# Kernel tuning notes

Measured on AMD Instinct MI355X. Metric: run time of the kernel, lower is better.

Reference implementation:

```python
import jax, jax.numpy as jnp
import numpy as np

N, D, E = 16384, 2048, 64   # tokens, d_model, num_experts
K = 9                        # self.k = min(k+1, num_experts) with k=8
EPS = 0.01
SIGMA = 1.0 / E              # Normal(0, 1/num_experts) stddev


def setup_inputs() -> dict:
    key = jax.random.key(0)
    ks = jax.random.split(key, 6)
    x = jax.random.normal(ks[0], (N, D), jnp.float32)
    Wr = jax.random.normal(ks[1], (D, E), jnp.float32) * 0.02
    br = jnp.zeros((E,), jnp.float32)
    Wn = jax.random.normal(ks[2], (D, E), jnp.float32) * 0.02
    bn = jnp.zeros((E,), jnp.float32)
    noise_eps = jax.random.normal(ks[3], (N, E), jnp.float32)
    # torch: (-empty.exponential_()).log() -> log of Exp(1) samples
    gumbel_noise = jnp.log(jax.random.exponential(ks[4], (N, E), jnp.float32))
    return {"x": x, "Wr": Wr, "br": br, "Wn": Wn, "bn": bn,
            "noise_eps": noise_eps, "gumbel_noise": gumbel_noise}


def reference(x, Wr, br, Wn, bn, noise_eps, gumbel_noise):
    raw_logits = x @ Wr + br                              # [N, E]
    noise_stddev = jax.nn.softplus(x @ Wn + bn) + EPS     # [N, E]
    noisy_logits = raw_logits + noise_eps * noise_stddev  # [N, E]

    top_vals, top_idx = jax.lax.top_k(noisy_logits, K)    # [N, K] sorted desc
    # scatter ones at top-k indices (indices unique per row)
    hard_mask = jax.nn.one_hot(top_idx, E, dtype=noisy_logits.dtype).sum(axis=1)  # [N, E]

    # gumbel-softmax straight-through relaxation
    mask_soft = jax.nn.softmax(noisy_logits + gumbel_noise, axis=-1)
    expert_mask = hard_mask - jax.lax.stop_gradient(mask_soft) + mask_soft

    route_prob = jax.nn.softmax(noisy_logits, axis=-1)    # [N, E]
    importance = jax.nn.softmax(raw_logits, axis=-1).sum(axis=0)  # [E]

    # load: P(raw + noise > threshold), Normal(0, 1/E) CDF per original
    threshold = top_vals[:, K - 1]                        # [N]
    z = (threshold[:, None] - raw_logits) / noise_stddev  # [N, E]
    cdf = 0.5 * (1.0 + jax.scipy.special.erf(z / (SIGMA * jnp.sqrt(jnp.float32(2.0)))))
    load = (1.0 - cdf).sum(axis=0)                        # [E]

    return (expert_mask, route_prob, importance, load)
```

## Files before the change

kernel.cpp:

```cpp
#include <hip/hip_runtime.h>
#include <hip/hip_bf16.h>
#include <math.h>

#define N_TOK 16384
#define DIM   2048
#define NE    64
#define TOPK  9

#define ROWS     32
#define DC       64
#define NCHUNK   (DIM / DC)
#define NTHREADS 256

typedef short  short8  __attribute__((ext_vector_type(8)));
typedef float  float4_ __attribute__((ext_vector_type(4)));
typedef unsigned short ushort_t;

__device__ __forceinline__ void async16(const void* g, void* l) {
    __builtin_amdgcn_global_load_lds(
        (const __attribute__((address_space(1))) void*)g,
        (__attribute__((address_space(3))) void*)l, 16, 0, 0);
}

__device__ __forceinline__ unsigned pk2(float a, float b) {
    float2 f; f.x = a; f.y = b;
    __hip_bfloat162 h = __float22bfloat162_rn(f);
    unsigned u;
    __builtin_memcpy(&u, &h, 4);
    return u;
}

__device__ __forceinline__ void cvt8(const float4_ va, const float4_ vb,
                                     short8* h, short8* l) {
    union { short8 s; unsigned u[4]; } H, L;
    const float f[8] = {va[0], va[1], va[2], va[3], vb[0], vb[1], vb[2], vb[3]};
#pragma unroll
    for (int i = 0; i < 4; ++i) {
        const float a = f[2 * i], b = f[2 * i + 1];
        const unsigned p = pk2(a, b);
        H.u[i] = p;
        const float ha = __uint_as_float(p << 16);
        const float hb = __uint_as_float(p & 0xffff0000u);
        L.u[i] = pk2(a - ha, b - hb);
    }
    *h = H.s; *l = L.s;
}

__device__ __forceinline__ float wave_max64(float v) {
#pragma unroll
    for (int off = 32; off > 0; off >>= 1)
        v = fmaxf(v, __shfl_xor(v, off, 64));
    return v;
}
__device__ __forceinline__ float wave_sum64(float v) {
#pragma unroll
    for (int off = 32; off > 0; off >>= 1)
        v += __shfl_xor(v, off, 64);
    return v;
}

__global__ __launch_bounds__(256)
void prep_w(const float* __restrict__ Wr, const float* __restrict__ Wn,
            ushort_t* __restrict__ wsW)
{
    const int gid = blockIdx.x * 256 + threadIdx.x;
    const int l   = gid & 63;
    const int ct  = (gid >> 6) & 7;
    const int kcg = gid >> 9;
    const int n   = ct * 16 + (l & 15);
    const int k0  = kcg * 32 + (l >> 4) * 8;
    const float* src = (n < NE) ? (Wr + n) : (Wn + (n - NE));
    union { short8 s; ushort_t us[8]; } H, L;
#pragma unroll
    for (int j = 0; j < 8; ++j) {
        const float v = src[(size_t)(k0 + j) * NE];
        const unsigned uv = __float_as_uint(v);
        const unsigned hb = (uv + 0x7fffu + ((uv >> 16) & 1u)) & 0xffff0000u;
        const float lo = v - __uint_as_float(hb);
        const unsigned ul = __float_as_uint(lo);
        H.us[j] = (ushort_t)(hb >> 16);
        L.us[j] = (ushort_t)((ul + 0x7fffu + ((ul >> 16) & 1u)) >> 16);
    }
    const size_t s0 = (size_t)(kcg * 8 + ct) * 2;
    *(short8*)(wsW + s0 * 512 + l * 8)         = H.s;
    *(short8*)(wsW + (s0 + 1) * 512 + l * 8)   = L.s;
}

__global__ __launch_bounds__(NTHREADS, 3)
void moe_main(const float* __restrict__ x,
              const float* __restrict__ br,
              const float* __restrict__ bn,
              const float* __restrict__ noise_eps,
              const float* __restrict__ gumbel,
              const ushort_t* __restrict__ wsW,
              float* __restrict__ out)
{
    __shared__ __align__(16) float smem[4352];

    const int t    = threadIdx.x;
    const int lane = t & 63;
    const int w    = t >> 6;
    const int c4   = lane & 15;
    const int q    = lane >> 4;
    const int row0 = blockIdx.x * ROWS;

    const float* gxp[2];
    int lxo[2];
#pragma unroll
    for (int ii = 0; ii < 2; ++ii) {
        const int i  = 2 * w + ii;
        const int r  = 4 * i + q;
        const int gk = c4 ^ (r & 15);
        gxp[ii] = x + (size_t)(row0 + r) * DIM + gk * 4;
        lxo[ii] = i * 256;
    }

    int aoff[2][2];
#pragma unroll
    for (int kc = 0; kc < 2; ++kc) {
        const int g0 = kc * 8 + q * 2;
        aoff[kc][0] = c4 * 64 + ((g0 ^ c4) * 4);
        aoff[kc][1] = c4 * 64 + (((g0 + 1) ^ c4) * 4);
    }

    float4_ acc[2][2];
#pragma unroll
    for (int rt = 0; rt < 2; ++rt)
#pragma unroll
        for (int cc = 0; cc < 2; ++cc)
            acc[rt][cc] = (float4_)(0.f);

    const char* wsB = (const char*)wsW;

#pragma unroll
    for (int ii = 0; ii < 2; ++ii) { async16(gxp[ii], &smem[lxo[ii]]); gxp[ii] += DC; }

    for (int ch = 0; ch < NCHUNK; ++ch) {
        __syncthreads();
        const int b = ch & 1;
        short8 bh[2][2], bl[2][2];
#pragma unroll
        for (int kc = 0; kc < 2; ++kc)
#pragma unroll
            for (int cc = 0; cc < 2; ++cc) {
                const size_t off = (size_t)(((ch * 2 + kc) * 8) + 2 * w + cc) * 2048 + lane * 16;
                bh[kc][cc] = *(const short8*)(wsB + off);
                bl[kc][cc] = *(const short8*)(wsB + off + 1024);
            }
        if (ch + 1 < NCHUNK) {
#pragma unroll
            for (int ii = 0; ii < 2; ++ii) {
                async16(gxp[ii], &smem[(b ^ 1) * 2048 + lxo[ii]]);
                gxp[ii] += DC;
            }
        }
        const float* xb = &smem[b * 2048];
#pragma unroll
        for (int kc = 0; kc < 2; ++kc)
#pragma unroll
            for (int rt = 0; rt < 2; ++rt) {
                const float4_ va = *(const float4_*)(xb + rt * 1024 + aoff[kc][0]);
                const float4_ vb = *(const float4_*)(xb + rt * 1024 + aoff[kc][1]);
                short8 ah, al;
                cvt8(va, vb, &ah, &al);
#pragma unroll
                for (int cc = 0; cc < 2; ++cc) {
                    acc[rt][cc] = __builtin_amdgcn_mfma_f32_16x16x32_bf16(ah, bh[kc][cc], acc[rt][cc], 0, 0, 0);
                    acc[rt][cc] = __builtin_amdgcn_mfma_f32_16x16x32_bf16(al, bh[kc][cc], acc[rt][cc], 0, 0, 0);
                    acc[rt][cc] = __builtin_amdgcn_mfma_f32_16x16x32_bf16(ah, bl[kc][cc], acc[rt][cc], 0, 0, 0);
                }
            }
    }

    __syncthreads();
    float* rawS = &smem[0];
    float* noiS = &smem[2080];
#pragma unroll
    for (int rt = 0; rt < 2; ++rt)
#pragma unroll
        for (int cc = 0; cc < 2; ++cc) {
            const int colg = (2 * w + cc) * 16 + c4;
            float* basep = (colg < NE) ? rawS : noiS;
            const int col = colg & 63;
#pragma unroll
            for (int v = 0; v < 4; ++v) {
                const int row = rt * 16 + q * 4 + v;
                basep[row * 65 + col] = acc[rt][cc][v];
            }
        }
    __syncthreads();

    const float br_l = br[lane];
    const float bn_l = bn[lane];
    float imp_acc = 0.f, load_acc = 0.f;
    float* out_em   = out;
    float* out_rp   = out + (size_t)N_TOK * NE;
    float* out_imp  = out + (size_t)2 * N_TOK * NE;
    float* out_load = out_imp + NE;

#pragma unroll 1
    for (int r = 0; r < 8; ++r) {
        const int lrow = w * 8 + r;
        const int row  = row0 + lrow;
        const float raw = rawS[lrow * 65 + lane] + br_l;
        const float nl  = noiS[lrow * 65 + lane] + bn_l;
        const float sd = fmaxf(nl, 0.f) + log1pf(expf(-fabsf(nl))) + 0.01f;
        const float epsv = noise_eps[(size_t)row * NE + lane];
        const float gum  = gumbel  [(size_t)row * NE + lane];
        const float noisy = fmaf(epsv, sd, raw);

        float cur = noisy;
        float thr = 0.f, m0 = 0.f;
#pragma unroll 1
        for (int k = 0; k < TOPK; ++k) {
            const float m = wave_max64(cur);
            if (k == 0) m0 = m;
            thr = m;
            const unsigned long long bm = __ballot(cur == m);
            const int first = __ffsll(bm) - 1;
            if (lane == first) cur = -INFINITY;
        }
        const float hard = (noisy >= thr) ? 1.f : 0.f;

        const float g  = noisy + gum;
        const float eg = expf(g - wave_max64(g));
        const float ms = eg / wave_sum64(eg);
        const float em = (hard - ms) + ms;

        const float en = expf(noisy - m0);
        const float rp = en / wave_sum64(en);

        const float er = expf(raw - wave_max64(raw));
        imp_acc += er / wave_sum64(er);

        const float z = (thr - raw) / sd;
        load_acc += 0.5f * erfcf(z * 45.254833995939045f);

        out_em[(size_t)row * NE + lane] = em;
        out_rp[(size_t)row * NE + lane] = rp;
    }

    __syncthreads();
    smem[w * 64 + lane]       = imp_acc;
    smem[256 + w * 64 + lane] = load_acc;
    __syncthreads();
    if (w == 0) {
        const float s1 = smem[lane] + smem[64 + lane] + smem[128 + lane] + smem[192 + lane];
        const float s2 = smem[256 + lane] + smem[320 + lane] + smem[384 + lane] + smem[448 + lane];
        atomicAdd(&out_imp[lane], s1);
        atomicAdd(&out_load[lane], s2);
    }
}

extern "C" void kernel_launch(void* const* d_in, const int* in_sizes, int n_in,
                              void* d_out, int out_size, void* d_ws, size_t ws_size,
                              hipStream_t stream)
{
    const float* x         = (const float*)d_in[0];
    const float* Wr        = (const float*)d_in[1];
    const float* br        = (const float*)d_in[2];
    const float* Wn        = (const float*)d_in[3];
    const float* bn        = (const float*)d_in[4];
    const float* noise_eps = (const float*)d_in[5];
    const float* gumbel    = (const float*)d_in[6];
    float* out = (float*)d_out;
    ushort_t* wsW = (ushort_t*)d_ws;

    (void)hipMemsetAsync((char*)d_out + (size_t)2 * N_TOK * NE * sizeof(float), 0,
                         2 * NE * sizeof(float), stream);
    prep_w<<<128, 256, 0, stream>>>(Wr, Wn, wsW);
    moe_main<<<N_TOK / ROWS, NTHREADS, 0, stream>>>(
        x, br, bn, noise_eps, gumbel, wsW, out);
}
```

Baseline: 266.9 us.

## Load x directly into registers with double-buffered prefetch instead of LDS staging

```diff
diff --git a/kernel.cpp b/kernel.cpp
--- a/kernel.cpp
+++ b/kernel.cpp
@@ -8,19 +8,13 @@
 #define TOPK  9
 
 #define ROWS     32
-#define DC       64
-#define NCHUNK   (DIM / DC)
+#define KC       32
+#define NSTEP    (DIM / KC)
 #define NTHREADS 256
 
 typedef short  short8  __attribute__((ext_vector_type(8)));
 typedef float  float4_ __attribute__((ext_vector_type(4)));
 typedef unsigned short ushort_t;
-
-__device__ __forceinline__ void async16(const void* g, void* l) {
-    __builtin_amdgcn_global_load_lds(
-        (const __attribute__((address_space(1))) void*)g,
-        (__attribute__((address_space(3))) void*)l, 16, 0, 0);
-}
 
 __device__ __forceinline__ unsigned pk2(float a, float b) {
     float2 f; f.x = a; f.y = b;
@@ -61,8 +55,10 @@
 
 __global__ __launch_bounds__(256)
 void prep_w(const float* __restrict__ Wr, const float* __restrict__ Wn,
-            ushort_t* __restrict__ wsW)
+            ushort_t* __restrict__ wsW, float* __restrict__ out)
 {
+    if (blockIdx.x == 0 && threadIdx.x < 2 * NE)
+        (out + (size_t)2 * N_TOK * NE)[threadIdx.x] = 0.f;
     const int gid = blockIdx.x * 256 + threadIdx.x;
     const int l   = gid & 63;
     const int ct  = (gid >> 6) & 7;
@@ -81,12 +77,12 @@
         H.us[j] = (ushort_t)(hb >> 16);
         L.us[j] = (ushort_t)((ul + 0x7fffu + ((ul >> 16) & 1u)) >> 16);
     }
-    const size_t s0 = (size_t)(kcg * 8 + ct) * 2;
-    *(short8*)(wsW + s0 * 512 + l * 8)         = H.s;
-    *(short8*)(wsW + (s0 + 1) * 512 + l * 8)   = L.s;
-}
-
-__global__ __launch_bounds__(NTHREADS, 3)
+    const size_t p = (size_t)(kcg * 8 + ct);
+    *(short8*)(wsW + p * 1024 + l * 8)        = H.s;
+    *(short8*)(wsW + p * 1024 + 512 + l * 8)  = L.s;
+}
+
+__global__ __launch_bounds__(NTHREADS, 2)
 void moe_main(const float* __restrict__ x,
               const float* __restrict__ br,
               const float* __restrict__ bn,
@@ -95,7 +91,7 @@
               const ushort_t* __restrict__ wsW,
               float* __restrict__ out)
 {
-    __shared__ __align__(16) float smem[4352];
+    __shared__ float smem[4160];
 
     const int t    = threadIdx.x;
     const int lane = t & 63;
@@ -104,24 +100,9 @@
     const int q    = lane >> 4;
     const int row0 = blockIdx.x * ROWS;
 
-    const float* gxp[2];
-    int lxo[2];
-#pragma unroll
-    for (int ii = 0; ii < 2; ++ii) {
-        const int i  = 2 * w + ii;
-        const int r  = 4 * i + q;
-        const int gk = c4 ^ (r & 15);
-        gxp[ii] = x + (size_t)(row0 + r) * DIM + gk * 4;
-        lxo[ii] = i * 256;
-    }
-
-    int aoff[2][2];
-#pragma unroll
-    for (int kc = 0; kc < 2; ++kc) {
-        const int g0 = kc * 8 + q * 2;
-        aoff[kc][0] = c4 * 64 + ((g0 ^ c4) * 4);
-        aoff[kc][1] = c4 * 64 + (((g0 + 1) ^ c4) * 4);
-    }
+    const float* x0 = x + (size_t)(row0 + c4)      * DIM + q * 8;
+    const float* x1 = x + (size_t)(row0 + 16 + c4) * DIM + q * 8;
+    const char* bbase = (const char*)wsW + (size_t)(2 * w) * 2048 + lane * 16;
 
     float4_ acc[2][2];
 #pragma unroll
@@ -130,49 +111,53 @@
         for (int cc = 0; cc < 2; ++cc)
             acc[rt][cc] = (float4_)(0.f);
 
-    const char* wsB = (const char*)wsW;
-
-#pragma unroll
-    for (int ii = 0; ii < 2; ++ii) { async16(gxp[ii], &smem[lxo[ii]]); gxp[ii] += DC; }
-
-    for (int ch = 0; ch < NCHUNK; ++ch) {
-        __syncthreads();
-        const int b = ch & 1;
-        short8 bh[2][2], bl[2][2];
-#pragma unroll
-        for (int kc = 0; kc < 2; ++kc)
-#pragma unroll
-            for (int cc = 0; cc < 2; ++cc) {
-                const size_t off = (size_t)(((ch * 2 + kc) * 8) + 2 * w + cc) * 2048 + lane * 16;
-                bh[kc][cc] = *(const short8*)(wsB + off);
-                bl[kc][cc] = *(const short8*)(wsB + off + 1024);
-            }
-        if (ch + 1 < NCHUNK) {
-#pragma unroll
-            for (int ii = 0; ii < 2; ++ii) {
-                async16(gxp[ii], &smem[(b ^ 1) * 2048 + lxo[ii]]);
-                gxp[ii] += DC;
-            }
-        }
-        const float* xb = &smem[b * 2048];
-#pragma unroll
-        for (int kc = 0; kc < 2; ++kc)
-#pragma unroll
-            for (int rt = 0; rt < 2; ++rt) {
-                const float4_ va = *(const float4_*)(xb + rt * 1024 + aoff[kc][0]);
-                const float4_ vb = *(const float4_*)(xb + rt * 1024 + aoff[kc][1]);
-                short8 ah, al;
-                cvt8(va, vb, &ah, &al);
-#pragma unroll
-                for (int cc = 0; cc < 2; ++cc) {
-                    acc[rt][cc] = __builtin_amdgcn_mfma_f32_16x16x32_bf16(ah, bh[kc][cc], acc[rt][cc], 0, 0, 0);
-                    acc[rt][cc] = __builtin_amdgcn_mfma_f32_16x16x32_bf16(al, bh[kc][cc], acc[rt][cc], 0, 0, 0);
-                    acc[rt][cc] = __builtin_amdgcn_mfma_f32_16x16x32_bf16(ah, bl[kc][cc], acc[rt][cc], 0, 0, 0);
-                }
-            }
-    }
-
-    __syncthreads();
+    float4_ pa[2][4];
+    short8  pb[2][4];
+#define LOAD_STEP(s_, buf_)  do {                                        \
+        const float* a0 = x0 + (s_) * KC;                                \
+        const float* a1 = x1 + (s_) * KC;                                \
+        pa[buf_][0] = *(const float4_*)(a0);                             \
+        pa[buf_][1] = *(const float4_*)(a0 + 4);                         \
+        pa[buf_][2] = *(const float4_*)(a1);                             \
+        pa[buf_][3] = *(const float4_*)(a1 + 4);                         \
+        const char* B = bbase + (size_t)(s_) * 16384;                    \
+        pb[buf_][0] = *(const short8*)(B);                               \
+        pb[buf_][1] = *(const short8*)(B + 1024);                        \
+        pb[buf_][2] = *(const short8*)(B + 2048);                        \
+        pb[buf_][3] = *(const short8*)(B + 3072);                        \
+    } while (0)
+#define COMPUTE_STEP(buf_) do {                                                              \
+        short8 ah, al;                                                                       \
+        const short8 bh0 = pb[buf_][0], bl0 = pb[buf_][1];                                   \
+        const short8 bh1 = pb[buf_][2], bl1 = pb[buf_][3];                                   \
+        cvt8(pa[buf_][0], pa[buf_][1], &ah, &al);                                            \
+        acc[0][0] = __builtin_amdgcn_mfma_f32_16x16x32_bf16(ah, bh0, acc[0][0], 0, 0, 0);    \
+        acc[0][0] = __builtin_amdgcn_mfma_f32_16x16x32_bf16(al, bh0, acc[0][0], 0, 0, 0);    \
+        acc[0][0] = __builtin_amdgcn_mfma_f32_16x16x32_bf16(ah, bl0, acc[0][0], 0, 0, 0);    \
+        acc[0][1] = __builtin_amdgcn_mfma_f32_16x16x32_bf16(ah, bh1, acc[0][1], 0, 0, 0);    \
+        acc[0][1] = __builtin_amdgcn_mfma_f32_16x16x32_bf16(al, bh1, acc[0][1], 0, 0, 0);    \
+        acc[0][1] = __builtin_amdgcn_mfma_f32_16x16x32_bf16(ah, bl1, acc[0][1], 0, 0, 0);    \
+        cvt8(pa[buf_][2], pa[buf_][3], &ah, &al);                                            \
+        acc[1][0] = __builtin_amdgcn_mfma_f32_16x16x32_bf16(ah, bh0, acc[1][0], 0, 0, 0);    \
+        acc[1][0] = __builtin_amdgcn_mfma_f32_16x16x32_bf16(al, bh0, acc[1][0], 0, 0, 0);    \
+        acc[1][0] = __builtin_amdgcn_mfma_f32_16x16x32_bf16(ah, bl0, acc[1][0], 0, 0, 0);    \
+        acc[1][1] = __builtin_amdgcn_mfma_f32_16x16x32_bf16(ah, bh1, acc[1][1], 0, 0, 0);    \
+        acc[1][1] = __builtin_amdgcn_mfma_f32_16x16x32_bf16(al, bh1, acc[1][1], 0, 0, 0);    \
+        acc[1][1] = __builtin_amdgcn_mfma_f32_16x16x32_bf16(ah, bl1, acc[1][1], 0, 0, 0);    \
+    } while (0)
+
+    LOAD_STEP(0, 0);
+    LOAD_STEP(1, 1);
+#pragma unroll 1
+    for (int s = 0; s < NSTEP - 2; s += 2) {
+        COMPUTE_STEP(0);
+        LOAD_STEP(s + 2, 0);
+        COMPUTE_STEP(1);
+        LOAD_STEP(s + 3, 1);
+    }
+    COMPUTE_STEP(0);
+    COMPUTE_STEP(1);
+
     float* rawS = &smem[0];
     float* noiS = &smem[2080];
 #pragma unroll
@@ -266,9 +251,7 @@
     float* out = (float*)d_out;
     ushort_t* wsW = (ushort_t*)d_ws;
 
-    (void)hipMemsetAsync((char*)d_out + (size_t)2 * N_TOK * NE * sizeof(float), 0,
-                         2 * NE * sizeof(float), stream);
-    prep_w<<<128, 256, 0, stream>>>(Wr, Wn, wsW);
+    prep_w<<<128, 256, 0, stream>>>(Wr, Wn, wsW, out);
     moe_main<<<N_TOK / ROWS, NTHREADS, 0, stream>>>(
         x, br, bn, noise_eps, gumbel, wsW, out);
 }
```

After: 280.3 us. 5.0% more time.
